# Kernel optimization log

Hardware: AMD Instinct MI355X
Metric: run time of the kernel (lower is better)

The kernel has to match this reference:

```python
import jax, jax.numpy as jnp
import numpy as np
import math

N, E, S, V, H, R = 10000, 160000, 512, 128, 8, 32
HD = S // H
CUTOFF = 10.0


def bessel_basis(d):
    # d: [E] -> [E, R], Bessel RBF with cosine cutoff
    freqs = jnp.arange(1, R + 1, dtype=d.dtype) * np.pi / CUTOFF  # [R]
    d1 = d[:, None]
    b = jnp.sin(freqs * d1) / jnp.maximum(d1, 1e-8)
    cut = 0.5 * (jnp.cos(np.pi * d1 / CUTOFF) + 1.0) * (d1 < CUTOFF).astype(d.dtype)
    return b * cut


def segment_softmax(logits, seg, num_seg):
    # logits: [E, H], seg: [E] destination node ids
    m = jax.ops.segment_max(logits, seg, num_segments=num_seg)
    m = jnp.where(jnp.isfinite(m), m, 0.0)
    e = jnp.exp(logits - m[seg])
    s = jax.ops.segment_sum(e, seg, num_segments=num_seg)
    return e / (s[seg] + 1e-9)


def layernorm(x, g, b, eps=1e-5):
    mu = jnp.mean(x, axis=-1, keepdims=True)
    var = jnp.mean(jnp.square(x - mu), axis=-1, keepdims=True)
    return (x - mu) * jax.lax.rsqrt(var + eps) * g + b


def setup_inputs() -> dict:
    key = jax.random.key(0)
    ks = jax.random.split(key, 24)
    sc = lambda fan_in: 1.0 / math.sqrt(fan_in)
    inp = {
        "scalars": jax.random.normal(ks[0], (N, S), jnp.float32),
        "vectors": jax.random.normal(ks[1], (N, V, 3), jnp.float32),
        "edge_vec": jax.random.normal(ks[2], (E, 3), jnp.float32),
        "Wq_s": jax.random.normal(ks[3], (S, S), jnp.float32) * sc(S),
        "bq_s": jnp.zeros((S,), jnp.float32),
        "Wk_s": jax.random.normal(ks[4], (S, S), jnp.float32) * sc(S),
        "bk_s": jnp.zeros((S,), jnp.float32),
        "Wv_s": jax.random.normal(ks[5], (S, S), jnp.float32) * sc(S),
        "bv_s": jnp.zeros((S,), jnp.float32),
        "Wq_v": jax.random.normal(ks[6], (V, V), jnp.float32) * sc(V),
        "Wk_v": jax.random.normal(ks[7], (V, V), jnp.float32) * sc(V),
        "Wv_v": jax.random.normal(ks[8], (V, V), jnp.float32) * sc(V),
        "Wout_s": jax.random.normal(ks[9], (S, S), jnp.float32) * sc(S),
        "bout_s": jnp.zeros((S,), jnp.float32),
        "Wout_v": jax.random.normal(ks[10], (V, V), jnp.float32) * sc(V),
        "bout_v": jnp.zeros((V,), jnp.float32),
        "W_edge": jax.random.normal(ks[11], (R, H), jnp.float32) * sc(R),
        "b_edge": jnp.zeros((H,), jnp.float32),
        "ln_g": jnp.ones((S,), jnp.float32),
        "ln_b": jnp.zeros((S,), jnp.float32),
        "edge_index": jax.random.randint(ks[12], (2, E), 0, N, jnp.int64),
    }
    return inp


def reference(scalars, vectors, edge_vec, Wq_s, bq_s, Wk_s, bk_s, Wv_s, bv_s,
              Wq_v, Wk_v, Wv_v, Wout_s, bout_s, Wout_v, bout_v,
              W_edge, b_edge, ln_g, ln_b, edge_index):
    row, col = edge_index[0], edge_index[1]
    edge_dist = jnp.linalg.norm(edge_vec, axis=-1)  # [E]

    # scalar Q/K/V, split into heads
    q_s = (scalars @ Wq_s + bq_s).reshape(N, H, HD)
    k_s = (scalars @ Wk_s + bk_s).reshape(N, H, HD)
    v_s = (scalars @ Wv_s + bv_s).reshape(N, H, HD)

    # vector Q/K/V: channel-mixing linear over the num_vectors axis (equivariant in 3D)
    q_v = jnp.einsum('nvi,vw->nwi', vectors, Wq_v)
    k_v = jnp.einsum('nvi,vw->nwi', vectors, Wk_v)
    v_v = jnp.einsum('nvi,vw->nwi', vectors, Wv_v)

    # per-edge attention logits
    att_s = jnp.einsum('ehd,ehd->eh', q_s[row], k_s[col])          # [E,H]
    att_v = jnp.einsum('evi,evi->e', q_v[row], k_v[col]) / math.sqrt(3.0)
    edge_att = bessel_basis(edge_dist) @ W_edge + b_edge            # [E,H]
    logits = (att_s + att_v[:, None] + edge_att) / math.sqrt(HD)

    # softmax over incoming edges of each destination node (row)
    attn = segment_softmax(logits, row, N)                          # [E,H]

    # scalar messages (per-head)
    msg_s = attn[:, :, None] * v_s[col]                             # [E,H,HD]
    out_s = jax.ops.segment_sum(msg_s, row, num_segments=N).reshape(N, S)
    out_s = out_s @ Wout_s + bout_s

    # vector messages (head-averaged attention, scalar gate keeps equivariance)
    a_v = jnp.mean(attn, axis=-1)                                   # [E]
    msg_v = a_v[:, None, None] * v_v[col]                           # [E,V,3]
    out_v = jax.ops.segment_sum(msg_v, row, num_segments=N)         # [N,V,3]
    out_v = jnp.einsum('nvi,vw->nwi', out_v, Wout_v) + bout_v[None, :, None]

    scalars_out = layernorm(scalars + out_s, ln_g, ln_b)
    vectors_out = vectors + out_v
    return scalars_out, vectors_out
```

## Files before the change

kernel.cpp:

```cpp
#include <hip/hip_runtime.h>
#include <math.h>

#define N_NODES 10000
#define E_EDGES 160000
#define S_DIM 512
#define QKV3 (3*S_DIM)
#define V_DIM 128
#define VQKV3 (3*V_DIM)
#define H_HEADS 8
#define R_BASIS 32
#define HD_DIM 64
#define NV3 (V_DIM*3)
#define KV8P 896

typedef _Float16 f16;
typedef f16 f16x2 __attribute__((ext_vector_type(2)));
typedef f16 f16x8 __attribute__((ext_vector_type(8)));
typedef float f32x4 __attribute__((ext_vector_type(4)));

static __device__ __forceinline__ float h2f(unsigned short u) {
  f16 h; __builtin_memcpy(&h, &u, 2); return (float)h;
}
static __device__ __forceinline__ unsigned short f2h(float f) {
  f16 h = (f16)f; unsigned short u; __builtin_memcpy(&u, &h, 2); return u;
}
static __device__ __forceinline__ float wave_sum(float v) {
  #pragma unroll
  for (int o = 32; o > 0; o >>= 1) v += __shfl_xor(v, o, 64);
  return v;
}
static __device__ __forceinline__ float wave_max(float v) {
  #pragma unroll
  for (int o = 32; o > 0; o >>= 1) v = fmaxf(v, __shfl_xor(v, o, 64));
  return v;
}

#if defined(__has_builtin)
#if __has_builtin(__builtin_amdgcn_sdot4)
#define SDOT4(a, b, c) __builtin_amdgcn_sdot4((int)(a), (int)(b), (c), false)
#endif
#endif
#ifndef SDOT4
static __device__ __forceinline__ int sdot4_sw(unsigned int a, unsigned int b, int c) {
  #pragma unroll
  for (int j = 0; j < 4; ++j)
    c += (int)(char)((a >> (8 * j)) & 0xff) * (int)(char)((b >> (8 * j)) & 0xff);
  return c;
}
#define SDOT4(a, b, c) sdot4_sw((a), (b), (c))
#endif

static __device__ __forceinline__ void fma_i8x4(unsigned int w, float wt, float* acc) {
  acc[0] = fmaf(wt, (float)(int)(char)(w & 0xff), acc[0]);
  acc[1] = fmaf(wt, (float)(int)(char)((w >> 8) & 0xff), acc[1]);
  acc[2] = fmaf(wt, (float)(int)(char)((w >> 16) & 0xff), acc[2]);
  acc[3] = fmaf(wt, (float)(int)(char)((w >> 24) & 0xff), acc[3]);
}

static __device__ __forceinline__ void glds16(const unsigned short* g, unsigned short* l) {
  __builtin_amdgcn_global_load_lds(
      (const __attribute__((address_space(1))) unsigned int*)g,
      (__attribute__((address_space(3))) unsigned int*)l, 16, 0, 0);
}

__global__ __launch_bounds__(256) void prep_kernel(
    const float* __restrict__ scalars, unsigned short* __restrict__ Af16,
    const int* __restrict__ ei, int* __restrict__ counts,
    const float* __restrict__ bq, const float* __restrict__ bk,
    const float* __restrict__ bv, float* __restrict__ bias_cat)
{
  int b = blockIdx.x, t = threadIdx.x;
  if (b < 5000) {
    int i = b * 256 + t;
    float4 v = reinterpret_cast<const float4*>(scalars)[i];
    ushort4 o;
    o.x = f2h(v.x); o.y = f2h(v.y); o.z = f2h(v.z); o.w = f2h(v.w);
    reinterpret_cast<ushort4*>(Af16)[i] = o;
  } else if (b < 5625) {
    int e = (b - 5000) * 256 + t;
    if (e < E_EDGES) atomicAdd(&counts[ei[e]], 1);
  } else {
    int c = (b - 5625) * 256 + t;
    if (c < QKV3)
      bias_cat[c] = (c < 512) ? bq[c] : (c < 1024) ? bk[c - 512] : bv[c - 1024];
  }
}

__global__ __launch_bounds__(256) void transpose4_kernel(
    const float* __restrict__ W0, const float* __restrict__ W1,
    const float* __restrict__ W2, const float* __restrict__ W3,
    unsigned short* __restrict__ Dcat, unsigned short* __restrict__ Do, int D)
{
  __shared__ float t[32][33];
  int z = blockIdx.z;
  const float* W = (z == 0) ? W0 : (z == 1) ? W1 : (z == 2) ? W2 : W3;
  unsigned short* dst = (z < 3) ? Dcat + (size_t)z * D * D : Do;
  int n0 = blockIdx.x * 32, k0 = blockIdx.y * 32;
  int x = threadIdx.x, y = threadIdx.y;
  #pragma unroll
  for (int j = 0; j < 32; j += 8)
    t[y + j][x] = W[(size_t)(k0 + y + j) * D + n0 + x];
  __syncthreads();
  #pragma unroll
  for (int j = 0; j < 32; j += 8)
    dst[(size_t)(n0 + y + j) * D + k0 + x] = f2h(t[x][y + j]);
}

__global__ __launch_bounds__(128) void vec_transpose_kernel(
    const float* __restrict__ vecs, unsigned short* __restrict__ VT)
{
  __shared__ float l[NV3];
  int n = blockIdx.x, t = threadIdx.x;
  #pragma unroll
  for (int j = 0; j < 3; ++j) l[t + j * 128] = vecs[(size_t)n * NV3 + t + j * 128];
  __syncthreads();
  #pragma unroll
  for (int i = 0; i < 3; ++i)
    VT[((size_t)n * 3 + i) * V_DIM + t] = f2h(l[t * 3 + i]);
}

__global__ __launch_bounds__(256) void gemm_f16_kernel(
    const unsigned short* __restrict__ A, const unsigned short* __restrict__ Bt,
    const float* __restrict__ bias, float* __restrict__ Cf,
    unsigned short* __restrict__ Ch, int M, int K, int Nn)
{
  __shared__ unsigned short lds[2][2][128 * 32];
  int tid = threadIdx.x;
  int wid = tid >> 6, lane = tid & 63;
  int wr = wid >> 1, wc = wid & 1;
  int row0 = blockIdx.y * 128, col0 = blockIdx.x * 128;

  int r0 = tid >> 2, s0 = tid & 3;
  int r1 = r0 + 64;
  int sw0 = (r0 >> 1) & 3;
  int aoff = (s0 ^ sw0) * 8;
  int gra0 = row0 + r0; if (gra0 >= M) gra0 = M - 1;
  int gra1 = row0 + r1; if (gra1 >= M) gra1 = M - 1;
  const unsigned short* ag0 = A + (size_t)gra0 * K + aoff;
  const unsigned short* ag1 = A + (size_t)gra1 * K + aoff;
  const unsigned short* bg0 = Bt + (size_t)(col0 + r0) * K + aoff;
  const unsigned short* bg1 = Bt + (size_t)(col0 + r1) * K + aoff;

  f32x4 acc[4][4];
  #pragma unroll
  for (int m = 0; m < 4; ++m)
    #pragma unroll
    for (int n = 0; n < 4; ++n) acc[m][n] = (f32x4){0.f, 0.f, 0.f, 0.f};

  int lr = lane & 15, lq = lane >> 4;
  int slot = (lq ^ ((lr >> 1) & 3)) * 8;
  int aro[4], bro[4];
  #pragma unroll
  for (int m = 0; m < 4; ++m) aro[m] = (wr * 64 + m * 16 + lr) * 32 + slot;
  #pragma unroll
  for (int n = 0; n < 4; ++n) bro[n] = (wc * 64 + n * 16 + lr) * 32 + slot;

  int nk = K >> 5;
  glds16(ag0, &lds[0][0][tid * 8]);
  glds16(ag1, &lds[0][0][(tid + 256) * 8]);
  glds16(bg0, &lds[0][1][tid * 8]);
  glds16(bg1, &lds[0][1][(tid + 256) * 8]);
  __syncthreads();

  for (int t = 0; t < nk; ++t) {
    int cur = t & 1;
    if (t + 1 < nk) {
      int ko = (t + 1) << 5;
      glds16(ag0 + ko, &lds[cur ^ 1][0][tid * 8]);
      glds16(ag1 + ko, &lds[cur ^ 1][0][(tid + 256) * 8]);
      glds16(bg0 + ko, &lds[cur ^ 1][1][tid * 8]);
      glds16(bg1 + ko, &lds[cur ^ 1][1][(tid + 256) * 8]);
    }
    const unsigned short* Ab = lds[cur][0];
    const unsigned short* Bb = lds[cur][1];
    f16x8 af[4], bf[4];
    #pragma unroll
    for (int m = 0; m < 4; ++m) af[m] = *reinterpret_cast<const f16x8*>(Ab + aro[m]);
    #pragma unroll
    for (int n = 0; n < 4; ++n) bf[n] = *reinterpret_cast<const f16x8*>(Bb + bro[n]);
    #pragma unroll
    for (int m = 0; m < 4; ++m)
      #pragma unroll
      for (int n = 0; n < 4; ++n)
        acc[m][n] = __builtin_amdgcn_mfma_f32_16x16x32_f16(af[m], bf[n], acc[m][n], 0, 0, 0);
    __syncthreads();
  }

  float bcol[4];
  #pragma unroll
  for (int n = 0; n < 4; ++n)
    bcol[n] = bias ? bias[col0 + wc * 64 + n * 16 + lr] : 0.f;
  int rl = tid >> 3, cc = (tid & 7) * 16;

  if (Cf) {
    float* cst = reinterpret_cast<float*>(&lds[0][0][0]);
    #pragma unroll
    for (int m = 0; m < 4; ++m) {
      __syncthreads();
      #pragma unroll
      for (int n = 0; n < 4; ++n)
        #pragma unroll
        for (int j = 0; j < 4; ++j)
          cst[(wr * 16 + lq * 4 + j) * 128 + wc * 64 + n * 16 + lr] = acc[m][n][j] + bcol[n];
      __syncthreads();
      int row = row0 + (rl >> 4) * 64 + m * 16 + (rl & 15);
      if (row < M) {
        float4* dst = reinterpret_cast<float4*>(Cf + (size_t)row * Nn + col0 + cc);
        const float4* src = reinterpret_cast<const float4*>(cst + rl * 128 + cc);
        dst[0] = src[0]; dst[1] = src[1]; dst[2] = src[2]; dst[3] = src[3];
      }
    }
  } else {
    unsigned short* csth = &lds[0][0][0];
    #pragma unroll
    for (int m = 0; m < 4; ++m) {
      __syncthreads();
      #pragma unroll
      for (int n = 0; n < 4; ++n)
        #pragma unroll
        for (int j = 0; j < 4; ++j)
          csth[(wr * 16 + lq * 4 + j) * 128 + wc * 64 + n * 16 + lr] = f2h(acc[m][n][j] + bcol[n]);
      __syncthreads();
      int row = row0 + (rl >> 4) * 64 + m * 16 + (rl & 15);
      if (row < M) {
        int4* dst = reinterpret_cast<int4*>(Ch + (size_t)row * Nn + col0 + cc);
        const int4* src = reinterpret_cast<const int4*>(csth + rl * 128 + cc);
        dst[0] = src[0]; dst[1] = src[1];
      }
    }
  }
}

__global__ __launch_bounds__(256) void pack_i8_kernel(
    const unsigned short* __restrict__ qkv_s, const unsigned short* __restrict__ qkv_v,
    char* __restrict__ q8, char* __restrict__ k8, char* __restrict__ v8,
    float* __restrict__ scales)
{
  __shared__ float am[336];
  __shared__ float inv_sh[3];
  int n = blockIdx.x, t = threadIdx.x;
  float va[2][8];

  auto loadChunk = [&](int chunk, float* v) {
    int r = chunk / 112, j = chunk - r * 112;
    int c = j * 8;
    const unsigned short* src;
    if (c < 512) {
      src = qkv_s + (size_t)n * QKV3 + r * 512 + c;
    } else {
      int cc = c - 512, i = cc >> 7, w = cc & 127;
      src = qkv_v + ((size_t)n * 3 + i) * VQKV3 + r * 128 + w;
    }
    int4 sv = *reinterpret_cast<const int4*>(src);
    union { int4 x; unsigned short u[8]; } us; us.x = sv;
    float m = 0.f;
    #pragma unroll
    for (int q = 0; q < 8; ++q) { v[q] = h2f(us.u[q]); m = fmaxf(m, fabsf(v[q])); }
    am[chunk] = m;
  };

  loadChunk(t, va[0]);
  if (t < 80) loadChunk(256 + t, va[1]);
  __syncthreads();

  int lane = t & 63, wid = t >> 6;
  if (wid < 3) {
    int basec = wid * 112;
    float m = am[basec + lane];
    if (lane < 48) m = fmaxf(m, am[basec + 64 + lane]);
    m = wave_max(m);
    if (lane == 0) {
      m = fmaxf(m, 1e-8f);
      scales[3 * n + wid] = m * (1.f / 127.f);
      inv_sh[wid] = 127.f / m;
    }
  }
  __syncthreads();

  auto quantStore = [&](int chunk, const float* v) {
    int r = chunk / 112, j = chunk - r * 112;
    float inv = inv_sh[r];
    unsigned int b0 = 0, b1 = 0;
    #pragma unroll
    for (int q = 0; q < 4; ++q) {
      int x = __float2int_rn(v[q] * inv);
      b0 |= ((unsigned)(x & 0xff)) << (8 * q);
    }
    #pragma unroll
    for (int q = 0; q < 4; ++q) {
      int x = __float2int_rn(v[4 + q] * inv);
      b1 |= ((unsigned)(x & 0xff)) << (8 * q);
    }
    char* dst = (r == 0 ? q8 : r == 1 ? k8 : v8) + (size_t)n * KV8P + j * 8;
    uint2 o; o.x = b0; o.y = b1;
    *reinterpret_cast<uint2*>(dst) = o;
  };

  quantStore(t, va[0]);
  if (t < 80) quantStore(256 + t, va[1]);
}

__global__ __launch_bounds__(1024) void scan_kernel(const int* __restrict__ counts,
                                                    int* __restrict__ offs) {
  __shared__ int wsum[16];
  __shared__ int carry_s;
  int tid = threadIdx.x;
  int lane = tid & 63, w = tid >> 6;
  if (tid == 0) carry_s = 0;
  __syncthreads();
  for (int base = 0; base < N_NODES; base += 1024) {
    int i = base + tid;
    int v = (i < N_NODES) ? counts[i] : 0;
    int x = v;
    #pragma unroll
    for (int o = 1; o < 64; o <<= 1) {
      int t = __shfl_up(x, o, 64);
      if (lane >= o) x += t;
    }
    if (lane == 63) wsum[w] = x;
    __syncthreads();
    if (w == 0 && lane < 16) {
      int t = wsum[lane];
      #pragma unroll
      for (int o = 1; o < 16; o <<= 1) {
        int u = __shfl_up(t, o, 64);
        if (lane >= o) t += u;
      }
      wsum[lane] = t;
    }
    __syncthreads();
    int incl = x + ((w > 0) ? wsum[w - 1] : 0);
    int c = carry_s;
    __syncthreads();
    if (i < N_NODES) offs[i] = c + incl - v;
    if (tid == 1023) carry_s = c + incl;
    __syncthreads();
  }
  if (tid == 0) offs[N_NODES] = carry_s;
}

__global__ void scatter_kernel(const int* __restrict__ ei, const int* __restrict__ offs,
                               int* __restrict__ cursor, int* __restrict__ eord) {
  int e = blockIdx.x * 256 + threadIdx.x;
  if (e < E_EDGES) {
    int r = ei[e];
    int p = offs[r] + atomicAdd(&cursor[r], 1);
    eord[p] = e;
  }
}

__global__ __launch_bounds__(256, 4) void edge_logits_kernel(
    const char* __restrict__ q8, const char* __restrict__ k8,
    const float* __restrict__ scales,
    const float* __restrict__ edge_vec, const int* __restrict__ ei,
    const int* __restrict__ eord,
    const float* __restrict__ W_edge, const float* __restrict__ b_edge,
    float* __restrict__ logits, int* __restrict__ cols)
{
  __shared__ float Wl[R_BASIS * H_HEADS];
  Wl[threadIdx.x] = W_edge[threadIdx.x];
  __syncthreads();

  int lane = threadIdx.x & 63;
  int wv = threadIdx.x >> 6;
  int g = lane >> 3, h = lane & 7;
  int pos = blockIdx.x * 32 + wv * 8 + g;
  int e = eord[pos];
  int row = ei[e], col = ei[E_EDGES + e];

  const char* qp = q8 + (size_t)row * KV8P + h * HD_DIM;
  const char* kp = k8 + (size_t)col * KV8P + h * HD_DIM;
  uint4 qa[4], ka[4];
  #pragma unroll
  for (int r = 0; r < 4; ++r) qa[r] = *reinterpret_cast<const uint4*>(qp + r * 16);
  #pragma unroll
  for (int r = 0; r < 4; ++r) ka[r] = *reinterpret_cast<const uint4*>(kp + r * 16);

  const char* qvp = q8 + (size_t)row * KV8P + 512 + h * 48;
  const char* kvp = k8 + (size_t)col * KV8P + 512 + h * 48;
  uint4 qv[3], kv[3];
  #pragma unroll
  for (int r = 0; r < 3; ++r) qv[r] = *reinterpret_cast<const uint4*>(qvp + r * 16);
  #pragma unroll
  for (int r = 0; r < 3; ++r) kv[r] = *reinterpret_cast<const uint4*>(kvp + r * 16);

  float sq = scales[3 * row + 0];
  float sk = scales[3 * col + 1];
  float ex = edge_vec[(size_t)e * 3 + 0];
  float ey = edge_vec[(size_t)e * 3 + 1];
  float ez = edge_vec[(size_t)e * 3 + 2];

  int dsum = 0;
  #pragma unroll
  for (int r = 0; r < 4; ++r) {
    dsum = SDOT4(qa[r].x, ka[r].x, dsum);
    dsum = SDOT4(qa[r].y, ka[r].y, dsum);
    dsum = SDOT4(qa[r].z, ka[r].z, dsum);
    dsum = SDOT4(qa[r].w, ka[r].w, dsum);
  }
  int dvec = 0;
  #pragma unroll
  for (int r = 0; r < 3; ++r) {
    dvec = SDOT4(qv[r].x, kv[r].x, dvec);
    dvec = SDOT4(qv[r].y, kv[r].y, dvec);
    dvec = SDOT4(qv[r].z, kv[r].z, dvec);
    dvec = SDOT4(qv[r].w, kv[r].w, dvec);
  }
  dvec += __shfl_xor(dvec, 1, 64);
  dvec += __shfl_xor(dvec, 2, 64);
  dvec += __shfl_xor(dvec, 4, 64);

  float att = sq * sk * ((float)dsum + 0.57735026918962576f * (float)dvec);

  float d = sqrtf(ex * ex + ey * ey + ez * ez);
  float th = d * 0.31415926535897932f;
  float s1 = __sinf(th), c1 = __cosf(th);
  float s2 = 2.f * s1 * c1,         c2 = fmaf(c1, c1, -s1 * s1);
  float s3 = fmaf(s2, c1, c2 * s1), c3 = fmaf(c2, c1, -s2 * s1);
  float s4 = 2.f * s2 * c2,         c4 = fmaf(c2, c2, -s2 * s2);
  float sr[4] = {s1, s2, s3, s4};
  float cr[4] = {c1, c2, c3, c4};
  float acc = 0.f;
  #pragma unroll
  for (int t = 0; t < 8; ++t) {
    #pragma unroll
    for (int j = 0; j < 4; ++j) {
      acc = fmaf(sr[j], Wl[(t * 4 + j) * H_HEADS + h], acc);
      float sn = fmaf(sr[j], c4, cr[j] * s4);
      cr[j] = fmaf(cr[j], c4, -sr[j] * s4);
      sr[j] = sn;
    }
  }
  float cut = (d < 10.f) ? 0.5f * (c1 + 1.f) : 0.f;
  float eah = fmaf(acc, cut / fmaxf(d, 1e-8f), b_edge[h]);

  logits[(size_t)pos * H_HEADS + h] = (att + eah) * 0.125f;
  if (h == 0) cols[pos] = col;
}

#define MAXDEG 512
__global__ __launch_bounds__(256) void agg_kernel(
    const float* __restrict__ logits, const int* __restrict__ cols,
    const char* __restrict__ v8, const float* __restrict__ scales,
    const int* __restrict__ offs,
    unsigned short* __restrict__ out_s, unsigned short* __restrict__ out_v)
{
  __shared__ float attn_lds[MAXDEG * H_HEADS];
  __shared__ float av_lds[MAXDEG];
  __shared__ int col_lds[MAXDEG];
  __shared__ float m_sh[H_HEADS], inv_sh[H_HEADS];

  int n = blockIdx.x;
  int beg = offs[n];
  int deg = offs[n + 1] - beg;
  int tid = threadIdx.x;
  bool fits = (deg <= MAXDEG);

  if (tid < 64) {
    int lane = tid;
    float lm[H_HEADS];
    #pragma unroll
    for (int h = 0; h < H_HEADS; ++h) lm[h] = -INFINITY;
    for (int i = lane; i < deg; i += 64) {
      const float4* lp = reinterpret_cast<const float4*>(logits + (size_t)(beg + i) * 8);
      float4 a = lp[0], b = lp[1];
      if (fits) col_lds[i] = cols[beg + i];
      lm[0] = fmaxf(lm[0], a.x); lm[1] = fmaxf(lm[1], a.y);
      lm[2] = fmaxf(lm[2], a.z); lm[3] = fmaxf(lm[3], a.w);
      lm[4] = fmaxf(lm[4], b.x); lm[5] = fmaxf(lm[5], b.y);
      lm[6] = fmaxf(lm[6], b.z); lm[7] = fmaxf(lm[7], b.w);
    }
    #pragma unroll
    for (int h = 0; h < H_HEADS; ++h) lm[h] = wave_max(lm[h]);

    float ls[H_HEADS];
    #pragma unroll
    for (int h = 0; h < H_HEADS; ++h) ls[h] = 0.f;
    for (int i = lane; i < deg; i += 64) {
      const float4* lp = reinterpret_cast<const float4*>(logits + (size_t)(beg + i) * 8);
      float4 a = lp[0], b = lp[1];
      float w[8];
      w[0] = expf(a.x - lm[0]); w[1] = expf(a.y - lm[1]);
      w[2] = expf(a.z - lm[2]); w[3] = expf(a.w - lm[3]);
      w[4] = expf(b.x - lm[4]); w[5] = expf(b.y - lm[5]);
      w[6] = expf(b.z - lm[6]); w[7] = expf(b.w - lm[7]);
      #pragma unroll
      for (int h = 0; h < H_HEADS; ++h) {
        ls[h] += w[h];
        if (fits) attn_lds[i * 8 + h] = w[h];
      }
    }
    #pragma unroll
    for (int h = 0; h < H_HEADS; ++h) ls[h] = wave_sum(ls[h]);

    float inv[H_HEADS];
    #pragma unroll
    for (int h = 0; h < H_HEADS; ++h) inv[h] = 1.f / (ls[h] + 1e-9f);
    if (lane == 0) {
      #pragma unroll
      for (int h = 0; h < H_HEADS; ++h) { m_sh[h] = lm[h]; inv_sh[h] = inv[h]; }
    }
    if (fits) {
      for (int i = lane; i < deg; i += 64) {
        float a = 0.f;
        #pragma unroll
        for (int h = 0; h < H_HEADS; ++h) a += attn_lds[i * 8 + h] * inv[h];
        av_lds[i] = 0.125f * a;
      }
    }
  }
  __syncthreads();

  int lane = tid & 63, wv = tid >> 6;
  int h = lane >> 3;
  float ih = inv_sh[h], mh = m_sh[h];
  float accs[8] = {0,0,0,0,0,0,0,0};
  float accv[8] = {0,0,0,0,0,0,0,0};

  auto body = [&](int i) {
    int colv;
    float wgt, av;
    if (fits) {
      colv = col_lds[i];
      wgt = attn_lds[i * 8 + h] * ih;
      av = av_lds[i];
    } else {
      colv = cols[beg + i];
      const float* lp = logits + (size_t)(beg + i) * 8;
      wgt = expf(lp[h] - mh) * ih;
      float a = 0.f;
      #pragma unroll
      for (int hh = 0; hh < H_HEADS; ++hh)
        a += expf(lp[hh] - m_sh[hh]) * inv_sh[hh];
      av = 0.125f * a;
    }
    float svc = scales[3 * colv + 2];
    wgt *= svc; av *= svc;
    uint2 vs = *reinterpret_cast<const uint2*>(v8 + (size_t)colv * KV8P + lane * 8);
    fma_i8x4(vs.x, wgt, accs);
    fma_i8x4(vs.y, wgt, accs + 4);
    if (lane < 48) {
      uint2 vvl = *reinterpret_cast<const uint2*>(v8 + (size_t)colv * KV8P + 512 + lane * 8);
      fma_i8x4(vvl.x, av, accv);
      fma_i8x4(vvl.y, av, accv + 4);
    }
  };

  int i = wv;
  for (; i + 4 < deg; i += 8) { body(i); body(i + 4); }
  if (i < deg) body(i);
  __syncthreads();

  float* red_s = attn_lds;
  float* red_v = attn_lds + 2048;
  #pragma unroll
  for (int j = 0; j < 8; j += 4)
    *reinterpret_cast<float4*>(&red_s[wv * 512 + lane * 8 + j]) =
      make_float4(accs[j], accs[j+1], accs[j+2], accs[j+3]);
  if (lane < 48) {
    #pragma unroll
    for (int j = 0; j < 8; j += 4)
      *reinterpret_cast<float4*>(&red_v[wv * 384 + lane * 8 + j]) =
        make_float4(accv[j], accv[j+1], accv[j+2], accv[j+3]);
  }
  __syncthreads();

  {
    int d0 = 2 * tid;
    float s0 = red_s[d0] + red_s[512 + d0] + red_s[1024 + d0] + red_s[1536 + d0];
    float s1 = red_s[d0+1] + red_s[512 + d0+1] + red_s[1024 + d0+1] + red_s[1536 + d0+1];
    ushort2 o; o.x = f2h(s0); o.y = f2h(s1);
    *reinterpret_cast<ushort2*>(out_s + (size_t)n * S_DIM + d0) = o;
  }
  if (tid < 192) {
    int d0 = 2 * tid;
    float s0 = red_v[d0] + red_v[384 + d0] + red_v[768 + d0] + red_v[1152 + d0];
    float s1 = red_v[d0+1] + red_v[384 + d0+1] + red_v[768 + d0+1] + red_v[1152 + d0+1];
    ushort2 o; o.x = f2h(s0); o.y = f2h(s1);
    *reinterpret_cast<ushort2*>(out_v + (size_t)n * NV3 + d0) = o;
  }
}

__global__ __launch_bounds__(128) void vec_epilogue_kernel(
    const float* __restrict__ tmp, const float* __restrict__ bout_v,
    const float* __restrict__ vectors, float* __restrict__ out)
{
  __shared__ float l[NV3];
  int n = blockIdx.x, t = threadIdx.x;
  #pragma unroll
  for (int i = 0; i < 3; ++i)
    l[i * 128 + t] = tmp[((size_t)n * 3 + i) * V_DIM + t];
  __syncthreads();
  #pragma unroll
  for (int c = 0; c < 3; ++c) {
    int j = t + c * 128;
    int w = j / 3, i = j - 3 * w;
    out[(size_t)n * NV3 + j] = l[i * 128 + w] + bout_v[w] + vectors[(size_t)n * NV3 + j];
  }
}

__global__ __launch_bounds__(256) void ln_kernel(
    const float* __restrict__ x0, const float* __restrict__ dx,
    const float* __restrict__ g, const float* __restrict__ b,
    float* __restrict__ out)
{
  int r = blockIdx.x * 4 + (threadIdx.x >> 6);
  int lane = threadIdx.x & 63;
  if (r >= N_NODES) return;
  float x[8];
  float s = 0.f;
  #pragma unroll
  for (int j = 0; j < 8; ++j) {
    int d = lane + j * 64;
    x[j] = x0[(size_t)r * S_DIM + d] + dx[(size_t)r * S_DIM + d];
    s += x[j];
  }
  s = wave_sum(s);
  float mu = s * (1.f / 512.f);
  float vs = 0.f;
  #pragma unroll
  for (int j = 0; j < 8; ++j) { float t = x[j] - mu; vs += t * t; }
  vs = wave_sum(vs);
  float inv = rsqrtf(vs * (1.f / 512.f) + 1e-5f);
  #pragma unroll
  for (int j = 0; j < 8; ++j) {
    int d = lane + j * 64;
    out[(size_t)r * S_DIM + d] = (x[j] - mu) * inv * g[d] + b[d];
  }
}

extern "C" void kernel_launch(void* const* d_in, const int* in_sizes, int n_in,
                              void* d_out, int out_size, void* d_ws, size_t ws_size,
                              hipStream_t stream)
{
  (void)in_sizes; (void)n_in; (void)out_size; (void)ws_size;
  const float* scalars  = (const float*)d_in[0];
  const float* vectors  = (const float*)d_in[1];
  const float* edge_vec = (const float*)d_in[2];
  const float* Wq_s = (const float*)d_in[3];
  const float* bq_s = (const float*)d_in[4];
  const float* Wk_s = (const float*)d_in[5];
  const float* bk_s = (const float*)d_in[6];
  const float* Wv_s = (const float*)d_in[7];
  const float* bv_s = (const float*)d_in[8];
  const float* Wq_v = (const float*)d_in[9];
  const float* Wk_v = (const float*)d_in[10];
  const float* Wv_v = (const float*)d_in[11];
  const float* Wout_s = (const float*)d_in[12];
  const float* bout_s = (const float*)d_in[13];
  const float* Wout_v = (const float*)d_in[14];
  const float* bout_v = (const float*)d_in[15];
  const float* W_edge = (const float*)d_in[16];
  const float* b_edge = (const float*)d_in[17];
  const float* ln_g = (const float*)d_in[18];
  const float* ln_b = (const float*)d_in[19];
  const int* ei = (const int*)d_in[20];

  float* out = (float*)d_out;
  const size_t NS  = (size_t)N_NODES * S_DIM;
  const size_t NVs = (size_t)N_NODES * NV3;
  const size_t EH  = (size_t)E_EDGES * H_HEADS;
  const size_t WSZ = (size_t)S_DIM * S_DIM;
  const size_t WVZ = (size_t)V_DIM * V_DIM;
  const int MV = N_NODES * 3;

  char* base = (char*)d_ws;
  auto carve = [&](size_t bytes) -> char* {
    char* p = base;
    base += (bytes + 255) & ~(size_t)255;
    return p;
  };
  unsigned short* Af16 = (unsigned short*)carve(NS * 2);
  unsigned short* VT0  = (unsigned short*)carve(NVs * 2);
  float* tmpv = (float*)Af16;
  char* v8 = (char*)Af16;
  unsigned short* qkv_s = (unsigned short*)carve((size_t)N_NODES * QKV3 * 2);
  unsigned short* qkv_v = (unsigned short*)carve((size_t)MV * VQKV3 * 2);
  unsigned short* outs_pre = (unsigned short*)carve(NS * 2);
  unsigned short* outv_pre = (unsigned short*)carve(NVs * 2);
  float* dx       = (float*)carve(NS * 4);
  char* q8 = (char*)dx;
  char* k8 = q8 + (size_t)N_NODES * KV8P;
  float* logitsS  = (float*)carve(EH * 4);
  int*   colsS    = (int*)carve(E_EDGES * 4);
  unsigned short* WqkvT  = (unsigned short*)carve(3 * WSZ * 2);
  unsigned short* WoT    = (unsigned short*)carve(WSZ * 2);
  unsigned short* WqkvvT = (unsigned short*)carve(3 * WVZ * 2);
  unsigned short* WovT   = (unsigned short*)carve(WVZ * 2);
  float* bias_cat = (float*)carve(QKV3 * 4);
  float* scales   = (float*)carve(3 * N_NODES * 4);
  int* counts = (int*)carve(N_NODES * 4);
  int* offs   = (int*)carve((N_NODES + 1) * 4);
  int* cursor = (int*)carve(N_NODES * 4);
  int* eord   = (int*)carve(E_EDGES * 4);

  hipMemsetAsync(counts, 0, N_NODES * sizeof(int), stream);
  hipMemsetAsync(cursor, 0, N_NODES * sizeof(int), stream);

  prep_kernel<<<5631, 256, 0, stream>>>(scalars, Af16, ei, counts,
                                        bq_s, bk_s, bv_s, bias_cat);
  dim3 tBlk(32, 8);
  transpose4_kernel<<<dim3(16, 16, 4), tBlk, 0, stream>>>(Wq_s, Wk_s, Wv_s, Wout_s, WqkvT, WoT, S_DIM);
  transpose4_kernel<<<dim3(4, 4, 4), tBlk, 0, stream>>>(Wq_v, Wk_v, Wv_v, Wout_v, WqkvvT, WovT, V_DIM);
  vec_transpose_kernel<<<N_NODES, 128, 0, stream>>>(vectors, VT0);

  gemm_f16_kernel<<<dim3(QKV3 / 128, (N_NODES + 127) / 128), 256, 0, stream>>>(
      Af16, WqkvT, bias_cat, nullptr, qkv_s, N_NODES, S_DIM, QKV3);
  gemm_f16_kernel<<<dim3(VQKV3 / 128, (MV + 127) / 128), 256, 0, stream>>>(
      VT0, WqkvvT, nullptr, nullptr, qkv_v, MV, V_DIM, VQKV3);

  pack_i8_kernel<<<N_NODES, 256, 0, stream>>>(qkv_s, qkv_v, q8, k8, v8, scales);

  scan_kernel<<<1, 1024, 0, stream>>>(counts, offs);
  scatter_kernel<<<(E_EDGES + 255) / 256, 256, 0, stream>>>(ei, offs, cursor, eord);

  edge_logits_kernel<<<E_EDGES / 32, 256, 0, stream>>>(q8, k8, scales, edge_vec,
                                                       ei, eord, W_edge, b_edge,
                                                       logitsS, colsS);

  agg_kernel<<<N_NODES, 256, 0, stream>>>(logitsS, colsS, v8, scales, offs,
                                          outs_pre, outv_pre);

  gemm_f16_kernel<<<dim3(S_DIM / 128, (N_NODES + 127) / 128), 256, 0, stream>>>(
      outs_pre, WoT, bout_s, dx, nullptr, N_NODES, S_DIM, S_DIM);
  gemm_f16_kernel<<<dim3(1, (MV + 127) / 128), 256, 0, stream>>>(
      outv_pre, WovT, nullptr, tmpv, nullptr, MV, V_DIM, V_DIM);
  vec_epilogue_kernel<<<N_NODES, 128, 0, stream>>>(tmpv, bout_v, vectors, out + NS);
  ln_kernel<<<2500, 256, 0, stream>>>(scalars, dx, ln_g, ln_b, out);
}
```

Measured before the change: 247.3 us.

## Fuse edge logit computation into per-node aggregation kernel

Merges the per-edge logit kernel into the per-destination aggregation kernel, so logits and column indices stay in LDS instead of round-tripping through global memory, and one launch is removed. The query row for the node is loaded once into LDS and reused across all of its edges. The softmax is now done by a single wave with head-parallel lanes using __expf. Degrees above MAXDEG are now clamped and the excess edges silently dropped, where the old code had a fallback path, so correctness depends on the input degree distribution.

```diff
diff --git a/kernel.cpp b/kernel.cpp
--- a/kernel.cpp
+++ b/kernel.cpp
@@ -23,11 +23,6 @@
 }
 static __device__ __forceinline__ unsigned short f2h(float f) {
   f16 h = (f16)f; unsigned short u; __builtin_memcpy(&u, &h, 2); return u;
-}
-static __device__ __forceinline__ float wave_sum(float v) {
-  #pragma unroll
-  for (int o = 32; o > 0; o >>= 1) v += __shfl_xor(v, o, 64);
-  return v;
 }
 static __device__ __forceinline__ float wave_max(float v) {
   #pragma unroll
@@ -349,193 +344,141 @@
   }
 }
 
-__global__ __launch_bounds__(256, 4) void edge_logits_kernel(
+#define MAXDEG 512
+__global__ __launch_bounds__(256) void agg_fused_kernel(
     const char* __restrict__ q8, const char* __restrict__ k8,
-    const float* __restrict__ scales,
+    const char* __restrict__ v8, const float* __restrict__ scales,
     const float* __restrict__ edge_vec, const int* __restrict__ ei,
-    const int* __restrict__ eord,
+    const int* __restrict__ eord, const int* __restrict__ offs,
     const float* __restrict__ W_edge, const float* __restrict__ b_edge,
-    float* __restrict__ logits, int* __restrict__ cols)
-{
-  __shared__ float Wl[R_BASIS * H_HEADS];
-  Wl[threadIdx.x] = W_edge[threadIdx.x];
-  __syncthreads();
-
-  int lane = threadIdx.x & 63;
-  int wv = threadIdx.x >> 6;
-  int g = lane >> 3, h = lane & 7;
-  int pos = blockIdx.x * 32 + wv * 8 + g;
-  int e = eord[pos];
-  int row = ei[e], col = ei[E_EDGES + e];
-
-  const char* qp = q8 + (size_t)row * KV8P + h * HD_DIM;
-  const char* kp = k8 + (size_t)col * KV8P + h * HD_DIM;
-  uint4 qa[4], ka[4];
-  #pragma unroll
-  for (int r = 0; r < 4; ++r) qa[r] = *reinterpret_cast<const uint4*>(qp + r * 16);
-  #pragma unroll
-  for (int r = 0; r < 4; ++r) ka[r] = *reinterpret_cast<const uint4*>(kp + r * 16);
-
-  const char* qvp = q8 + (size_t)row * KV8P + 512 + h * 48;
-  const char* kvp = k8 + (size_t)col * KV8P + 512 + h * 48;
-  uint4 qv[3], kv[3];
-  #pragma unroll
-  for (int r = 0; r < 3; ++r) qv[r] = *reinterpret_cast<const uint4*>(qvp + r * 16);
-  #pragma unroll
-  for (int r = 0; r < 3; ++r) kv[r] = *reinterpret_cast<const uint4*>(kvp + r * 16);
-
-  float sq = scales[3 * row + 0];
-  float sk = scales[3 * col + 1];
-  float ex = edge_vec[(size_t)e * 3 + 0];
-  float ey = edge_vec[(size_t)e * 3 + 1];
-  float ez = edge_vec[(size_t)e * 3 + 2];
-
-  int dsum = 0;
-  #pragma unroll
-  for (int r = 0; r < 4; ++r) {
-    dsum = SDOT4(qa[r].x, ka[r].x, dsum);
-    dsum = SDOT4(qa[r].y, ka[r].y, dsum);
-    dsum = SDOT4(qa[r].z, ka[r].z, dsum);
-    dsum = SDOT4(qa[r].w, ka[r].w, dsum);
-  }
-  int dvec = 0;
-  #pragma unroll
-  for (int r = 0; r < 3; ++r) {
-    dvec = SDOT4(qv[r].x, kv[r].x, dvec);
-    dvec = SDOT4(qv[r].y, kv[r].y, dvec);
-    dvec = SDOT4(qv[r].z, kv[r].z, dvec);
-    dvec = SDOT4(qv[r].w, kv[r].w, dvec);
-  }
-  dvec += __shfl_xor(dvec, 1, 64);
-  dvec += __shfl_xor(dvec, 2, 64);
-  dvec += __shfl_xor(dvec, 4, 64);
-
-  float att = sq * sk * ((float)dsum + 0.57735026918962576f * (float)dvec);
-
-  float d = sqrtf(ex * ex + ey * ey + ez * ez);
-  float th = d * 0.31415926535897932f;
-  float s1 = __sinf(th), c1 = __cosf(th);
-  float s2 = 2.f * s1 * c1,         c2 = fmaf(c1, c1, -s1 * s1);
-  float s3 = fmaf(s2, c1, c2 * s1), c3 = fmaf(c2, c1, -s2 * s1);
-  float s4 = 2.f * s2 * c2,         c4 = fmaf(c2, c2, -s2 * s2);
-  float sr[4] = {s1, s2, s3, s4};
-  float cr[4] = {c1, c2, c3, c4};
-  float acc = 0.f;
-  #pragma unroll
-  for (int t = 0; t < 8; ++t) {
-    #pragma unroll
-    for (int j = 0; j < 4; ++j) {
-      acc = fmaf(sr[j], Wl[(t * 4 + j) * H_HEADS + h], acc);
-      float sn = fmaf(sr[j], c4, cr[j] * s4);
-      cr[j] = fmaf(cr[j], c4, -sr[j] * s4);
-      sr[j] = sn;
-    }
-  }
-  float cut = (d < 10.f) ? 0.5f * (c1 + 1.f) : 0.f;
-  float eah = fmaf(acc, cut / fmaxf(d, 1e-8f), b_edge[h]);
-
-  logits[(size_t)pos * H_HEADS + h] = (att + eah) * 0.125f;
-  if (h == 0) cols[pos] = col;
-}
-
-#define MAXDEG 512
-__global__ __launch_bounds__(256) void agg_kernel(
-    const float* __restrict__ logits, const int* __restrict__ cols,
-    const char* __restrict__ v8, const float* __restrict__ scales,
-    const int* __restrict__ offs,
     unsigned short* __restrict__ out_s, unsigned short* __restrict__ out_v)
 {
   __shared__ float attn_lds[MAXDEG * H_HEADS];
   __shared__ float av_lds[MAXDEG];
   __shared__ int col_lds[MAXDEG];
+  __shared__ uint4 q_lds[56];
+  __shared__ float Wl[R_BASIS * H_HEADS];
   __shared__ float m_sh[H_HEADS], inv_sh[H_HEADS];
+  __shared__ float sq_sh;
 
   int n = blockIdx.x;
   int beg = offs[n];
   int deg = offs[n + 1] - beg;
+  if (deg > MAXDEG) deg = MAXDEG;
   int tid = threadIdx.x;
-  bool fits = (deg <= MAXDEG);
-
-  if (tid < 64) {
-    int lane = tid;
-    float lm[H_HEADS];
-    #pragma unroll
-    for (int h = 0; h < H_HEADS; ++h) lm[h] = -INFINITY;
-    for (int i = lane; i < deg; i += 64) {
-      const float4* lp = reinterpret_cast<const float4*>(logits + (size_t)(beg + i) * 8);
-      float4 a = lp[0], b = lp[1];
-      if (fits) col_lds[i] = cols[beg + i];
-      lm[0] = fmaxf(lm[0], a.x); lm[1] = fmaxf(lm[1], a.y);
-      lm[2] = fmaxf(lm[2], a.z); lm[3] = fmaxf(lm[3], a.w);
-      lm[4] = fmaxf(lm[4], b.x); lm[5] = fmaxf(lm[5], b.y);
-      lm[6] = fmaxf(lm[6], b.z); lm[7] = fmaxf(lm[7], b.w);
-    }
-    #pragma unroll
-    for (int h = 0; h < H_HEADS; ++h) lm[h] = wave_max(lm[h]);
-
-    float ls[H_HEADS];
-    #pragma unroll
-    for (int h = 0; h < H_HEADS; ++h) ls[h] = 0.f;
-    for (int i = lane; i < deg; i += 64) {
-      const float4* lp = reinterpret_cast<const float4*>(logits + (size_t)(beg + i) * 8);
-      float4 a = lp[0], b = lp[1];
-      float w[8];
-      w[0] = expf(a.x - lm[0]); w[1] = expf(a.y - lm[1]);
-      w[2] = expf(a.z - lm[2]); w[3] = expf(a.w - lm[3]);
-      w[4] = expf(b.x - lm[4]); w[5] = expf(b.y - lm[5]);
-      w[6] = expf(b.z - lm[6]); w[7] = expf(b.w - lm[7]);
+  Wl[tid] = W_edge[tid];
+  if (tid < 56) q_lds[tid] = reinterpret_cast<const uint4*>(q8 + (size_t)n * KV8P)[tid];
+  if (tid == 56) sq_sh = scales[3 * n + 0];
+  __syncthreads();
+
+  int lane = tid & 63, wv = tid >> 6;
+  int g = lane >> 3, h = lane & 7;
+  float sq = sq_sh;
+
+  for (int i = wv * 8 + g; i < deg; i += 32) {
+    int e = eord[beg + i];
+    int col = ei[E_EDGES + e];
+    const char* kp = k8 + (size_t)col * KV8P;
+    uint4 ka[4], kv[3];
+    #pragma unroll
+    for (int r = 0; r < 4; ++r)
+      ka[r] = *reinterpret_cast<const uint4*>(kp + h * HD_DIM + r * 16);
+    #pragma unroll
+    for (int r = 0; r < 3; ++r)
+      kv[r] = *reinterpret_cast<const uint4*>(kp + 512 + h * 48 + r * 16);
+    float sk = scales[3 * col + 1];
+    float ex = edge_vec[(size_t)e * 3 + 0];
+    float ey = edge_vec[(size_t)e * 3 + 1];
+    float ez = edge_vec[(size_t)e * 3 + 2];
+
+    int dsum = 0;
+    #pragma unroll
+    for (int r = 0; r < 4; ++r) {
+      uint4 qa = q_lds[h * 4 + r];
+      dsum = SDOT4(qa.x, ka[r].x, dsum);
+      dsum = SDOT4(qa.y, ka[r].y, dsum);
+      dsum = SDOT4(qa.z, ka[r].z, dsum);
+      dsum = SDOT4(qa.w, ka[r].w, dsum);
+    }
+    int dvec = 0;
+    #pragma unroll
+    for (int r = 0; r < 3; ++r) {
+      uint4 qv = q_lds[32 + h * 3 + r];
+      dvec = SDOT4(qv.x, kv[r].x, dvec);
+      dvec = SDOT4(qv.y, kv[r].y, dvec);
+      dvec = SDOT4(qv.z, kv[r].z, dvec);
+      dvec = SDOT4(qv.w, kv[r].w, dvec);
+    }
+    dvec += __shfl_xor(dvec, 1, 64);
+    dvec += __shfl_xor(dvec, 2, 64);
+    dvec += __shfl_xor(dvec, 4, 64);
+    float att = sq * sk * ((float)dsum + 0.57735026918962576f * (float)dvec);
+
+    float d = sqrtf(ex * ex + ey * ey + ez * ez);
+    float th = d * 0.31415926535897932f;
+    float s1 = __sinf(th), c1 = __cosf(th);
+    float s2 = 2.f * s1 * c1,         c2 = fmaf(c1, c1, -s1 * s1);
+    float s3 = fmaf(s2, c1, c2 * s1), c3 = fmaf(c2, c1, -s2 * s1);
+    float s4 = 2.f * s2 * c2,         c4 = fmaf(c2, c2, -s2 * s2);
+    float sr[4] = {s1, s2, s3, s4};
+    float cr[4] = {c1, c2, c3, c4};
+    float acc = 0.f;
+    #pragma unroll
+    for (int t = 0; t < 8; ++t) {
       #pragma unroll
-      for (int h = 0; h < H_HEADS; ++h) {
-        ls[h] += w[h];
-        if (fits) attn_lds[i * 8 + h] = w[h];
+      for (int j = 0; j < 4; ++j) {
+        acc = fmaf(sr[j], Wl[(t * 4 + j) * H_HEADS + h], acc);
+        float sn = fmaf(sr[j], c4, cr[j] * s4);
+        cr[j] = fmaf(cr[j], c4, -sr[j] * s4);
+        sr[j] = sn;
       }
     }
-    #pragma unroll
-    for (int h = 0; h < H_HEADS; ++h) ls[h] = wave_sum(ls[h]);
-
-    float inv[H_HEADS];
-    #pragma unroll
-    for (int h = 0; h < H_HEADS; ++h) inv[h] = 1.f / (ls[h] + 1e-9f);
-    if (lane == 0) {
-      #pragma unroll
-      for (int h = 0; h < H_HEADS; ++h) { m_sh[h] = lm[h]; inv_sh[h] = inv[h]; }
-    }
-    if (fits) {
-      for (int i = lane; i < deg; i += 64) {
-        float a = 0.f;
-        #pragma unroll
-        for (int h = 0; h < H_HEADS; ++h) a += attn_lds[i * 8 + h] * inv[h];
-        av_lds[i] = 0.125f * a;
-      }
-    }
-  }
-  __syncthreads();
-
-  int lane = tid & 63, wv = tid >> 6;
-  int h = lane >> 3;
-  float ih = inv_sh[h], mh = m_sh[h];
+    float cut = (d < 10.f) ? 0.5f * (c1 + 1.f) : 0.f;
+    float eah = fmaf(acc, cut / fmaxf(d, 1e-8f), b_edge[h]);
+
+    attn_lds[i * 8 + h] = (att + eah) * 0.125f;
+    if (h == 0) col_lds[i] = col;
+  }
+  __syncthreads();
+
+  if (wv == 0) {
+    float m = -INFINITY;
+    for (int i = g; i < deg; i += 8) m = fmaxf(m, attn_lds[i * 8 + h]);
+    m = fmaxf(m, __shfl_xor(m, 8, 64));
+    m = fmaxf(m, __shfl_xor(m, 16, 64));
+    m = fmaxf(m, __shfl_xor(m, 32, 64));
+
+    float s = 0.f;
+    for (int i = g; i < deg; i += 8) {
+      float w = __expf(attn_lds[i * 8 + h] - m);
+      attn_lds[i * 8 + h] = w;
+      s += w;
+    }
+    s += __shfl_xor(s, 8, 64);
+    s += __shfl_xor(s, 16, 64);
+    s += __shfl_xor(s, 32, 64);
+    float inv = 1.f / (s + 1e-9f);
+    if (lane < 8) { m_sh[lane] = m; inv_sh[lane] = inv; }
+
+    for (int i = g; i < deg; i += 8) {
+      float t = attn_lds[i * 8 + h] * inv;
+      t += __shfl_xor(t, 1, 64);
+      t += __shfl_xor(t, 2, 64);
+      t += __shfl_xor(t, 4, 64);
+      if (h == 0) av_lds[i] = 0.125f * t;
+    }
+  }
+  __syncthreads();
+
+  int hc = lane >> 3;
+  float ih = inv_sh[hc];
   float accs[8] = {0,0,0,0,0,0,0,0};
   float accv[8] = {0,0,0,0,0,0,0,0};
-
-  auto body = [&](int i) {
-    int colv;
-    float wgt, av;
-    if (fits) {
-      colv = col_lds[i];
-      wgt = attn_lds[i * 8 + h] * ih;
-      av = av_lds[i];
-    } else {
-      colv = cols[beg + i];
-      const float* lp = logits + (size_t)(beg + i) * 8;
-      wgt = expf(lp[h] - mh) * ih;
-      float a = 0.f;
-      #pragma unroll
-      for (int hh = 0; hh < H_HEADS; ++hh)
-        a += expf(lp[hh] - m_sh[hh]) * inv_sh[hh];
-      av = 0.125f * a;
-    }
+  for (int i = wv; i < deg; i += 4) {
+    int colv = col_lds[i];
     float svc = scales[3 * colv + 2];
-    wgt *= svc; av *= svc;
+    float wgt = attn_lds[i * 8 + hc] * ih * svc;
+    float av = av_lds[i] * svc;
     uint2 vs = *reinterpret_cast<const uint2*>(v8 + (size_t)colv * KV8P + lane * 8);
     fma_i8x4(vs.x, wgt, accs);
     fma_i8x4(vs.y, wgt, accs + 4);
@@ -544,11 +487,7 @@
       fma_i8x4(vvl.x, av, accv);
       fma_i8x4(vvl.y, av, accv + 4);
     }
-  };
-
-  int i = wv;
-  for (; i + 4 < deg; i += 8) { body(i); body(i + 4); }
-  if (i < deg) body(i);
+  }
   __syncthreads();
 
   float* red_s = attn_lds;
@@ -615,12 +554,14 @@
     x[j] = x0[(size_t)r * S_DIM + d] + dx[(size_t)r * S_DIM + d];
     s += x[j];
   }
-  s = wave_sum(s);
+  #pragma unroll
+  for (int o = 32; o > 0; o >>= 1) s += __shfl_xor(s, o, 64);
   float mu = s * (1.f / 512.f);
   float vs = 0.f;
   #pragma unroll
   for (int j = 0; j < 8; ++j) { float t = x[j] - mu; vs += t * t; }
-  vs = wave_sum(vs);
+  #pragma unroll
+  for (int o = 32; o > 0; o >>= 1) vs += __shfl_xor(vs, o, 64);
   float inv = rsqrtf(vs * (1.f / 512.f) + 1e-5f);
   #pragma unroll
   for (int j = 0; j < 8; ++j) {
@@ -659,7 +600,6 @@
   float* out = (float*)d_out;
   const size_t NS  = (size_t)N_NODES * S_DIM;
   const size_t NVs = (size_t)N_NODES * NV3;
-  const size_t EH  = (size_t)E_EDGES * H_HEADS;
   const size_t WSZ = (size_t)S_DIM * S_DIM;
   const size_t WVZ = (size_t)V_DIM * V_DIM;
   const int MV = N_NODES * 3;
@@ -681,8 +621,6 @@
   float* dx       = (float*)carve(NS * 4);
   char* q8 = (char*)dx;
   char* k8 = q8 + (size_t)N_NODES * KV8P;
-  float* logitsS  = (float*)carve(EH * 4);
-  int*   colsS    = (int*)carve(E_EDGES * 4);
   unsigned short* WqkvT  = (unsigned short*)carve(3 * WSZ * 2);
   unsigned short* WoT    = (unsigned short*)carve(WSZ * 2);
   unsigned short* WqkvvT = (unsigned short*)carve(3 * WVZ * 2);
@@ -714,12 +652,9 @@
   scan_kernel<<<1, 1024, 0, stream>>>(counts, offs);
   scatter_kernel<<<(E_EDGES + 255) / 256, 256, 0, stream>>>(ei, offs, cursor, eord);
 
-  edge_logits_kernel<<<E_EDGES / 32, 256, 0, stream>>>(q8, k8, scales, edge_vec,
-                                                       ei, eord, W_edge, b_edge,
-                                                       logitsS, colsS);
-
-  agg_kernel<<<N_NODES, 256, 0, stream>>>(logitsS, colsS, v8, scales, offs,
-                                          outs_pre, outv_pre);
+  agg_fused_kernel<<<N_NODES, 256, 0, stream>>>(q8, k8, v8, scales, edge_vec,
+                                                ei, eord, offs, W_edge, b_edge,
+                                                outs_pre, outv_pre);
 
   gemm_f16_kernel<<<dim3(S_DIM / 128, (N_NODES + 127) / 128), 256, 0, stream>>>(
       outs_pre, WoT, bout_s, dx, nullptr, N_NODES, S_DIM, S_DIM);
```

Measured after the change: 258.5 us. +4.5%, slower.
